# Kernel tuning notes

Measured on AMD Instinct MI355X. Metric: run time of the kernel, lower is better.

Reference implementation:

```python
import jax, jax.numpy as jnp
import numpy as np

N, E = 50000, 800000
IN, HID, H, C = 128, 64, 4, 2
NEG_SLOPE = 0.2


def _gat_layer(h, src, dst, W, al, ar, b, out_dim, residual, resW=None, act='elu'):
    # h: [N, in]; W: [H*out, in]; al/ar: [H, out]; b: [H*out]
    n = h.shape[0]
    feat = (h @ W.T).reshape(n, H, out_dim)            # [N, H, out]
    el = jnp.einsum('nho,ho->nh', feat, al)            # [N, H]
    er = jnp.einsum('nho,ho->nh', feat, ar)            # [N, H]
    e = jax.nn.leaky_relu(el[src] + er[dst], NEG_SLOPE)  # [E, H]
    # segment softmax over incoming edges of each dst node
    emax = jax.ops.segment_max(e, dst, num_segments=n)
    ee = jnp.exp(e - emax[dst])
    denom = jax.ops.segment_sum(ee, dst, num_segments=n)
    alpha = ee / denom[dst]                             # [E, H]
    msg = feat[src] * alpha[:, :, None]                 # [E, H, out]
    rst = jax.ops.segment_sum(msg, dst, num_segments=n)  # [N, H, out]
    if residual == 'id':
        rst = rst + h.reshape(n, H, out_dim)
    elif residual == 'fc':
        rst = rst + (h @ resW.T).reshape(n, H, out_dim)
    rst = rst + b.reshape(1, H, out_dim)
    if act == 'elu':
        rst = jax.nn.elu(rst)
    else:  # softmax over last dim (F.softmax)
        rst = jax.nn.softmax(rst, axis=-1)
    return rst


def setup_inputs() -> dict:
    key = jax.random.key(0)
    ks = jax.random.split(key, 24)
    x = jax.random.normal(ks[0], (N, IN), dtype=jnp.float32)
    src = jax.random.randint(ks[1], (E,), 0, N)
    dst = jax.random.randint(ks[2], (E,), 0, N)
    s = 0.1
    d = {'x': x, 'src': src, 'dst': dst}
    # layer 1: IN -> (H, HID), no residual
    d['W1'] = jax.random.normal(ks[3], (H * HID, IN), dtype=jnp.float32) * s
    d['al1'] = jax.random.normal(ks[4], (H, HID), dtype=jnp.float32) * s
    d['ar1'] = jax.random.normal(ks[5], (H, HID), dtype=jnp.float32) * s
    d['b1'] = jnp.zeros((H * HID,), dtype=jnp.float32)
    # layers 2,3: H*HID -> (H, HID), identity residual
    d['W2'] = jax.random.normal(ks[6], (H * HID, H * HID), dtype=jnp.float32) * s
    d['al2'] = jax.random.normal(ks[7], (H, HID), dtype=jnp.float32) * s
    d['ar2'] = jax.random.normal(ks[8], (H, HID), dtype=jnp.float32) * s
    d['b2'] = jnp.zeros((H * HID,), dtype=jnp.float32)
    d['W3'] = jax.random.normal(ks[9], (H * HID, H * HID), dtype=jnp.float32) * s
    d['al3'] = jax.random.normal(ks[10], (H, HID), dtype=jnp.float32) * s
    d['ar3'] = jax.random.normal(ks[11], (H, HID), dtype=jnp.float32) * s
    d['b3'] = jnp.zeros((H * HID,), dtype=jnp.float32)
    # layer 4: H*HID -> (H, C), linear residual, softmax activation, mean over heads
    d['W4'] = jax.random.normal(ks[12], (H * C, H * HID), dtype=jnp.float32) * s
    d['al4'] = jax.random.normal(ks[13], (H, C), dtype=jnp.float32) * s
    d['ar4'] = jax.random.normal(ks[14], (H, C), dtype=jnp.float32) * s
    d['b4'] = jnp.zeros((H * C,), dtype=jnp.float32)
    d['resW4'] = jax.random.normal(ks[15], (H * C, H * HID), dtype=jnp.float32) * s
    return d


def reference(x, src, dst, W1, al1, ar1, b1, W2, al2, ar2, b2, W3, al3, ar3, b3, W4, al4, ar4, b4, resW4):
    h = _gat_layer(x, src, dst, W1, al1, ar1, b1, HID, 'none', act='elu').reshape(N, H * HID)
    h = _gat_layer(h, src, dst, W2, al2, ar2, b2, HID, 'id', act='elu').reshape(N, H * HID)
    h = _gat_layer(h, src, dst, W3, al3, ar3, b3, HID, 'id', act='elu').reshape(N, H * HID)
    h = _gat_layer(h, src, dst, W4, al4, ar4, b4, C, 'fc', resW=resW4, act='softmax')
    return h.mean(axis=1)  # [N, C]
```

## Files before the change

kernel.cpp:

```cpp
#include <hip/hip_runtime.h>
#include <hip/hip_bf16.h>
#include <math.h>


#define LEAKY_SLOPE 0.2f

typedef __bf16 bf16x8_t __attribute__((ext_vector_type(8)));
typedef float f32x4_t __attribute__((ext_vector_type(4)));
typedef float f32x2_t __attribute__((ext_vector_type(2)));

__device__ __forceinline__ float leaky(float x) { return x > 0.f ? x : LEAKY_SLOPE * x; }
__device__ __forceinline__ float eluf(float x)  { return x > 0.f ? x : expm1f(x); }
__device__ __forceinline__ float bflo(unsigned u) { return __uint_as_float(u << 16); }
__device__ __forceinline__ float bfhi(unsigned u) { return __uint_as_float(u & 0xffff0000u); }

__device__ __forceinline__ int rli(int v, int l) { return __builtin_amdgcn_readlane(v, l); }
__device__ __forceinline__ float rlf(float v, int l) {
  return __uint_as_float((unsigned)__builtin_amdgcn_readlane((int)__float_as_uint(v), l));
}
template <int CTRL>
__device__ __forceinline__ float dpp_add(float x) {
  int t = __builtin_amdgcn_update_dpp(0, (int)__float_as_uint(x), CTRL, 0xf, 0xf, false);
  return x + __uint_as_float((unsigned)t);
}
__device__ __forceinline__ float wsum_dpp(float x) {
  x = dpp_add<0x111>(x);
  x = dpp_add<0x112>(x);
  x = dpp_add<0x114>(x);
  x = dpp_add<0x118>(x);
  x = dpp_add<0x142>(x);
  x = dpp_add<0x143>(x);
  return rlf(x, 63);
}
__device__ __forceinline__ float rowsum_dpp(float x) {
  x = dpp_add<0x111>(x);
  x = dpp_add<0x112>(x);
  x = dpp_add<0x114>(x);
  x = dpp_add<0x118>(x);
  return x;
}
__device__ __forceinline__ float wmax(float v) {
#pragma unroll
  for (int o = 32; o; o >>= 1) v = fmaxf(v, __shfl_xor(v, o));
  return v;
}
__device__ __forceinline__ float wsum_sh(float v) {
#pragma unroll
  for (int o = 32; o; o >>= 1) v += __shfl_xor(v, o);
  return v;
}

__device__ __forceinline__ void edge_fma(f32x2_t& a01, f32x2_t& a23, uint2 u, float4 w) {
  f32x2_t f01 = {bflo(u.x), bfhi(u.x)};
  f32x2_t f23 = {bflo(u.y), bfhi(u.y)};
  f32x2_t w01 = {w.x, w.y};
  f32x2_t w23 = {w.z, w.w};
  a01 = __builtin_elementwise_fma(w01, f01, a01);
  a23 = __builtin_elementwise_fma(w23, f23, a23);
}

__device__ __forceinline__ void gl_lds16(const __hip_bfloat16* g, __bf16* l) {
  __builtin_amdgcn_global_load_lds((const __attribute__((address_space(1))) void*)g,
                                   (__attribute__((address_space(3))) void*)l, 16, 0, 0);
}

__global__ __launch_bounds__(1024) void scan1_k(const int* __restrict__ deg,
                                                int* __restrict__ rowp,
                                                int* __restrict__ bsum, int n) {
  __shared__ int sd[1024];
  int tid = threadIdx.x;
  int i = blockIdx.x * 1024 + tid;
  int v = (i < n) ? deg[i] : 0;
  int x = v;
  sd[tid] = x;
  __syncthreads();
  for (int off = 1; off < 1024; off <<= 1) {
    int t = (tid >= off) ? sd[tid - off] : 0;
    __syncthreads();
    x += t;
    sd[tid] = x;
    __syncthreads();
  }
  if (i < n) rowp[i] = x - v;
  if (tid == 1023) bsum[blockIdx.x] = x;
}

__global__ void scan23_k(const int* __restrict__ bsum, int* __restrict__ rowp, int n, int nb) {
  __shared__ int pref[65];
  int tid = threadIdx.x;
  if (tid < 64) {
    int v = (tid < nb) ? bsum[tid] : 0;
    int x = v;
#pragma unroll
    for (int off = 1; off < 64; off <<= 1) {
      int t = __shfl_up(x, off);
      if (tid >= off) x += t;
    }
    pref[tid] = x - v;
    if (tid == 63) pref[64] = x;
  }
  __syncthreads();
  int i = blockIdx.x * 256 + tid;
  if (i < n) rowp[i] += pref[i >> 10];
  if (i == n) rowp[n] = pref[64];
}

__global__ void scatter_k(const int* __restrict__ src, const int* __restrict__ dst,
                          const int* __restrict__ rowp, int* __restrict__ cur,
                          int* __restrict__ csrc, int e) {
  int i = blockIdx.x * 256 + threadIdx.x;
  if (i < e) {
    int d = dst[i];
    int p = atomicAdd(&cur[d], 1);
    csrc[rowp[d] + p] = src[i];
  }
}

__global__ void cvthist_k(const float* __restrict__ x, const float* __restrict__ W1,
                          const float* __restrict__ W2, const float* __restrict__ W3,
                          const float* __restrict__ W4, const float* __restrict__ rW4,
                          __hip_bfloat16* __restrict__ xb, __hip_bfloat16* __restrict__ W1b,
                          __hip_bfloat16* __restrict__ W2b, __hip_bfloat16* __restrict__ W3b,
                          __hip_bfloat16* __restrict__ Wcatb, int nx,
                          const int* __restrict__ dst, int* __restrict__ deg, int e) {
  int i = blockIdx.x * 256 + threadIdx.x;
  if (i < e) atomicAdd(&deg[dst[i]], 1);
  if (i < nx) { xb[i] = __float2bfloat16(x[i]); return; }
  int j = i - nx;
  if (j < 32768) W1b[j] = __float2bfloat16(W1[j]);
  else if (j < 98304)  { int k = j - 32768;  W2b[k] = __float2bfloat16(W2[k]); }
  else if (j < 163840) { int k = j - 98304;  W3b[k] = __float2bfloat16(W3[k]); }
  else if (j < 165888) { int k = j - 163840; Wcatb[k] = __float2bfloat16(W4[k]); }
  else if (j < 167936) { int k = j - 165888; Wcatb[2048 + k] = __float2bfloat16(rW4[k]); }
}

template <int K>
__global__ __launch_bounds__(256) void gemm_mfma(const __hip_bfloat16* __restrict__ A,
                                                 const __hip_bfloat16* __restrict__ B,
                                                 __hip_bfloat16* __restrict__ featb,
                                                 const float* __restrict__ al,
                                                 const float* __restrict__ ar,
                                                 float* __restrict__ el,
                                                 float* __restrict__ er, int n) {
  __shared__ __bf16 As[128 * 32];
  __shared__ __bf16 Bs[128 * 32];
  const int tid = threadIdx.x;
  const int lane = tid & 63, w = tid >> 6;
  const int tm = lane & 15, tq = lane >> 4;
  const int wm = (w & 1) * 64, wn = (w >> 1) * 64;
  const int r0 = blockIdx.x * 128, c0 = blockIdx.y * 128;

  f32x4_t acc[4][4];
#pragma unroll
  for (int i = 0; i < 4; ++i)
#pragma unroll
    for (int j = 0; j < 4; ++j) acc[i][j] = 0.f;

  const bool interior = (r0 + 128 <= n);
  if (interior) {
    const int srow = w * 32 + (lane >> 2);
    const int scol = (lane & 3) * 8;
    for (int kk = 0; kk < K; kk += 32) {
      __syncthreads();
      const __hip_bfloat16* ga = A + (size_t)(r0 + srow) * K + kk + scol;
      const __hip_bfloat16* gb = B + (size_t)(c0 + srow) * K + kk + scol;
      gl_lds16(ga, As + w * 1024);
      gl_lds16(ga + (size_t)16 * K, As + w * 1024 + 512);
      gl_lds16(gb, Bs + w * 1024);
      gl_lds16(gb + (size_t)16 * K, Bs + w * 1024 + 512);
      __syncthreads();
      bf16x8_t af[4], bfr[4];
#pragma unroll
      for (int i = 0; i < 4; ++i) af[i] = *(const bf16x8_t*)&As[(wm + i * 16 + tm) * 32 + tq * 8];
#pragma unroll
      for (int j = 0; j < 4; ++j) bfr[j] = *(const bf16x8_t*)&Bs[(wn + j * 16 + tm) * 32 + tq * 8];
#pragma unroll
      for (int i = 0; i < 4; ++i)
#pragma unroll
        for (int j = 0; j < 4; ++j)
          acc[i][j] = __builtin_amdgcn_mfma_f32_16x16x32_bf16(af[i], bfr[j], acc[i][j], 0, 0, 0);
    }
  } else {
    const int srow = tid >> 1, sko = (tid & 1) * 16;
    for (int kk = 0; kk < K; kk += 32) {
      uint4 av0 = {0, 0, 0, 0}, av1 = {0, 0, 0, 0};
      int arw = r0 + srow;
      if (arw < n) {
        const uint4* p = (const uint4*)(A + (size_t)arw * K + kk + sko);
        av0 = p[0];
        av1 = p[1];
      }
      const uint4* q = (const uint4*)(B + (size_t)(c0 + srow) * K + kk + sko);
      uint4 bv0 = q[0], bv1 = q[1];
      __syncthreads();
      *(uint4*)&As[srow * 32 + sko] = av0;
      *(uint4*)&As[srow * 32 + sko + 8] = av1;
      *(uint4*)&Bs[srow * 32 + sko] = bv0;
      *(uint4*)&Bs[srow * 32 + sko + 8] = bv1;
      __syncthreads();
      bf16x8_t af[4], bfr[4];
#pragma unroll
      for (int i = 0; i < 4; ++i) af[i] = *(const bf16x8_t*)&As[(wm + i * 16 + tm) * 32 + tq * 8];
#pragma unroll
      for (int j = 0; j < 4; ++j) bfr[j] = *(const bf16x8_t*)&Bs[(wn + j * 16 + tm) * 32 + tq * 8];
#pragma unroll
      for (int i = 0; i < 4; ++i)
#pragma unroll
        for (int j = 0; j < 4; ++j)
          acc[i][j] = __builtin_amdgcn_mfma_f32_16x16x32_bf16(af[i], bfr[j], acc[i][j], 0, 0, 0);
    }
  }

#pragma unroll
  for (int i = 0; i < 4; ++i) {
#pragma unroll
    for (int j = 0; j < 4; ++j) {
      int col = c0 + wn + j * 16 + tm;
      int hh = col >> 6, oo = col & 63;
#pragma unroll
      for (int rr = 0; rr < 4; ++rr) {
        int row = r0 + wm + i * 16 + tq * 4 + rr;
        if (row < n) featb[(size_t)row * 256 + oo * 4 + hh] = __float2bfloat16(acc[i][j][rr]);
      }
    }
  }

  {
    const int hd = (c0 + wn) >> 6;
    float alv[4], arv[4];
#pragma unroll
    for (int j = 0; j < 4; ++j) {
      alv[j] = al[hd * 64 + j * 16 + tm];
      arv[j] = ar[hd * 64 + j * 16 + tm];
    }
#pragma unroll
    for (int i = 0; i < 4; ++i) {
#pragma unroll
      for (int rr = 0; rr < 4; ++rr) {
        float se = acc[i][0][rr] * alv[0] + acc[i][1][rr] * alv[1] +
                   acc[i][2][rr] * alv[2] + acc[i][3][rr] * alv[3];
        float sr2 = acc[i][0][rr] * arv[0] + acc[i][1][rr] * arv[1] +
                    acc[i][2][rr] * arv[2] + acc[i][3][rr] * arv[3];
        se = rowsum_dpp(se);
        sr2 = rowsum_dpp(sr2);
        if (tm == 15) {
          int row = r0 + wm + i * 16 + tq * 4 + rr;
          if (row < n) {
            el[(size_t)row * 4 + hd] = se;
            er[(size_t)row * 4 + hd] = sr2;
          }
        }
      }
    }
  }
}

template <int RES>
__global__ __launch_bounds__(256) void agg64_k(const __hip_bfloat16* __restrict__ featb,
                                               const float* __restrict__ el,
                                               const float* __restrict__ er,
                                               const int* __restrict__ rowp,
                                               const int* __restrict__ csrc,
                                               const __hip_bfloat16* __restrict__ hinb,
                                               const float* __restrict__ bias,
                                               __hip_bfloat16* __restrict__ houtb, int n) {
  __shared__ float wsh[4][256];
  int wv = threadIdx.x >> 6;
  int node = blockIdx.x * 4 + wv;
  int lane = threadIdx.x & 63;
  if (node >= n) return;
  int s0 = rowp[node], s1 = rowp[node + 1];
  int deg = s1 - s0;
  float4 erv = *(const float4*)(er + (size_t)node * 4);
  f32x2_t a01 = {0.f, 0.f}, a23 = {0.f, 0.f};

  if (deg <= 64) {
    int sown = 0;
    float x0 = 0.f, x1 = 0.f, x2 = 0.f, x3 = 0.f;
    if (lane < deg) {
      sown = csrc[s0 + lane];
      float4 e = *(const float4*)(el + (size_t)sown * 4);
      x0 = __expf(leaky(e.x + erv.x));
      x1 = __expf(leaky(e.y + erv.y));
      x2 = __expf(leaky(e.z + erv.z));
      x3 = __expf(leaky(e.w + erv.w));
    }
    float d0 = wsum_dpp(x0), d1 = wsum_dpp(x1), d2 = wsum_dpp(x2), d3 = wsum_dpp(x3);
    float i0 = d0 > 0.f ? 1.f / d0 : 0.f;
    float i1 = d1 > 0.f ? 1.f / d1 : 0.f;
    float i2 = d2 > 0.f ? 1.f / d2 : 0.f;
    float i3 = d3 > 0.f ? 1.f / d3 : 0.f;
    float4 wq = {x0 * i0, x1 * i1, x2 * i2, x3 * i3};
    *(float4*)&wsh[wv][lane * 4] = wq;

    int k = 0;
    for (; k + 8 <= deg; k += 8) {
      int sk0 = rli(sown, k + 0), sk1 = rli(sown, k + 1);
      int sk2 = rli(sown, k + 2), sk3 = rli(sown, k + 3);
      int sk4 = rli(sown, k + 4), sk5 = rli(sown, k + 5);
      int sk6 = rli(sown, k + 6), sk7 = rli(sown, k + 7);
      uint2 u0 = ((const uint2*)(featb + ((size_t)sk0 << 8)))[lane];
      uint2 u1 = ((const uint2*)(featb + ((size_t)sk1 << 8)))[lane];
      uint2 u2 = ((const uint2*)(featb + ((size_t)sk2 << 8)))[lane];
      uint2 u3 = ((const uint2*)(featb + ((size_t)sk3 << 8)))[lane];
      uint2 u4 = ((const uint2*)(featb + ((size_t)sk4 << 8)))[lane];
      uint2 u5 = ((const uint2*)(featb + ((size_t)sk5 << 8)))[lane];
      uint2 u6 = ((const uint2*)(featb + ((size_t)sk6 << 8)))[lane];
      uint2 u7 = ((const uint2*)(featb + ((size_t)sk7 << 8)))[lane];
      edge_fma(a01, a23, u0, *(const float4*)&wsh[wv][(k + 0) * 4]);
      edge_fma(a01, a23, u1, *(const float4*)&wsh[wv][(k + 1) * 4]);
      edge_fma(a01, a23, u2, *(const float4*)&wsh[wv][(k + 2) * 4]);
      edge_fma(a01, a23, u3, *(const float4*)&wsh[wv][(k + 3) * 4]);
      edge_fma(a01, a23, u4, *(const float4*)&wsh[wv][(k + 4) * 4]);
      edge_fma(a01, a23, u5, *(const float4*)&wsh[wv][(k + 5) * 4]);
      edge_fma(a01, a23, u6, *(const float4*)&wsh[wv][(k + 6) * 4]);
      edge_fma(a01, a23, u7, *(const float4*)&wsh[wv][(k + 7) * 4]);
    }
    for (; k + 4 <= deg; k += 4) {
      int sk0 = rli(sown, k + 0), sk1 = rli(sown, k + 1);
      int sk2 = rli(sown, k + 2), sk3 = rli(sown, k + 3);
      uint2 u0 = ((const uint2*)(featb + ((size_t)sk0 << 8)))[lane];
      uint2 u1 = ((const uint2*)(featb + ((size_t)sk1 << 8)))[lane];
      uint2 u2 = ((const uint2*)(featb + ((size_t)sk2 << 8)))[lane];
      uint2 u3 = ((const uint2*)(featb + ((size_t)sk3 << 8)))[lane];
      edge_fma(a01, a23, u0, *(const float4*)&wsh[wv][(k + 0) * 4]);
      edge_fma(a01, a23, u1, *(const float4*)&wsh[wv][(k + 1) * 4]);
      edge_fma(a01, a23, u2, *(const float4*)&wsh[wv][(k + 2) * 4]);
      edge_fma(a01, a23, u3, *(const float4*)&wsh[wv][(k + 3) * 4]);
    }
    for (; k < deg; ++k) {
      int sk = rli(sown, k);
      uint2 u = ((const uint2*)(featb + ((size_t)sk << 8)))[lane];
      edge_fma(a01, a23, u, *(const float4*)&wsh[wv][k * 4]);
    }
  } else {
    float m0 = -INFINITY, m1 = -INFINITY, m2 = -INFINITY, m3 = -INFINITY;
    for (int k = s0 + lane; k < s1; k += 64) {
      int s = csrc[k];
      float4 e = *(const float4*)(el + (size_t)s * 4);
      m0 = fmaxf(m0, leaky(e.x + erv.x));
      m1 = fmaxf(m1, leaky(e.y + erv.y));
      m2 = fmaxf(m2, leaky(e.z + erv.z));
      m3 = fmaxf(m3, leaky(e.w + erv.w));
    }
    m0 = wmax(m0); m1 = wmax(m1); m2 = wmax(m2); m3 = wmax(m3);
    float d0 = 0, d1 = 0, d2 = 0, d3 = 0;
    for (int k = s0 + lane; k < s1; k += 64) {
      int s = csrc[k];
      float4 e = *(const float4*)(el + (size_t)s * 4);
      d0 += __expf(leaky(e.x + erv.x) - m0);
      d1 += __expf(leaky(e.y + erv.y) - m1);
      d2 += __expf(leaky(e.z + erv.z) - m2);
      d3 += __expf(leaky(e.w + erv.w) - m3);
    }
    d0 = wsum_sh(d0); d1 = wsum_sh(d1); d2 = wsum_sh(d2); d3 = wsum_sh(d3);
    float j0 = d0 > 0.f ? 1.f / d0 : 0.f;
    float j1 = d1 > 0.f ? 1.f / d1 : 0.f;
    float j2 = d2 > 0.f ? 1.f / d2 : 0.f;
    float j3 = d3 > 0.f ? 1.f / d3 : 0.f;
    for (int k = s0; k < s1; ++k) {
      int s = csrc[k];
      float4 e = *(const float4*)(el + (size_t)s * 4);
      float4 wk;
      wk.x = __expf(leaky(e.x + erv.x) - m0) * j0;
      wk.y = __expf(leaky(e.y + erv.y) - m1) * j1;
      wk.z = __expf(leaky(e.z + erv.z) - m2) * j2;
      wk.w = __expf(leaky(e.w + erv.w) - m3) * j3;
      uint2 u = ((const uint2*)(featb + ((size_t)s << 8)))[lane];
      edge_fma(a01, a23, u, wk);
    }
  }

  size_t base = (size_t)node * 256;
  float v0 = a01[0] + bias[lane];
  float v1 = a01[1] + bias[64 + lane];
  float v2 = a23[0] + bias[128 + lane];
  float v3 = a23[1] + bias[192 + lane];
  if (RES) {
    v0 += __bfloat162float(hinb[base + lane]);
    v1 += __bfloat162float(hinb[base + 64 + lane]);
    v2 += __bfloat162float(hinb[base + 128 + lane]);
    v3 += __bfloat162float(hinb[base + 192 + lane]);
  }
  houtb[base + lane]       = __float2bfloat16(eluf(v0));
  houtb[base + 64 + lane]  = __float2bfloat16(eluf(v1));
  houtb[base + 128 + lane] = __float2bfloat16(eluf(v2));
  houtb[base + 192 + lane] = __float2bfloat16(eluf(v3));
}

__global__ __launch_bounds__(256) void l4mfma_k(const __hip_bfloat16* __restrict__ hb,
                                                const __hip_bfloat16* __restrict__ Wcat,
                                                const float* __restrict__ al4,
                                                const float* __restrict__ ar4,
                                                float* __restrict__ feat4,
                                                float* __restrict__ res4,
                                                float* __restrict__ el4,
                                                float* __restrict__ er4, int n) {
  int wid = blockIdx.x * 4 + (threadIdx.x >> 6);
  int n16 = (n + 15) >> 4;
  if (wid >= n16) return;
  int lane = threadIdx.x & 63;
  int tm = lane & 15, tq = lane >> 4;
  int row = wid * 16 + tm;
  int rowc = row < n ? row : n - 1;
  const __hip_bfloat16* ap = hb + (size_t)rowc * 256 + tq * 8;
  const __hip_bfloat16* bp = Wcat + (size_t)tm * 256 + tq * 8;
  f32x4_t acc = {0.f, 0.f, 0.f, 0.f};
#pragma unroll
  for (int k = 0; k < 8; ++k) {
    bf16x8_t af = *(const bf16x8_t*)(ap + k * 32);
    bf16x8_t bf = *(const bf16x8_t*)(bp + k * 32);
    acc = __builtin_amdgcn_mfma_f32_16x16x32_bf16(af, bf, acc, 0, 0, 0);
  }
  float* dstp = (tm < 8) ? feat4 : res4;
  int cc = tm & 7;
  float a4 = (tm < 8) ? al4[tm] : 0.f;
  float r4 = (tm < 8) ? ar4[tm] : 0.f;
#pragma unroll
  for (int r = 0; r < 4; ++r) {
    int node = wid * 16 + tq * 4 + r;
    float te = acc[r] * a4;
    float tr = acc[r] * r4;
    te += __shfl_xor(te, 1);
    tr += __shfl_xor(tr, 1);
    if (node < n) {
      dstp[(size_t)node * 8 + cc] = acc[r];
      if (tm < 8 && (tm & 1) == 0) {
        el4[(size_t)node * 4 + (tm >> 1)] = te;
        er4[(size_t)node * 4 + (tm >> 1)] = tr;
      }
    }
  }
}

__global__ __launch_bounds__(256) void agg4_k(const float* __restrict__ feat4,
                                              const float* __restrict__ el4,
                                              const float* __restrict__ er4,
                                              const int* __restrict__ rowp,
                                              const int* __restrict__ csrc,
                                              const float* __restrict__ res4,
                                              const float* __restrict__ b4,
                                              float* __restrict__ out, int n) {
  __shared__ int ssh[4][64];
  __shared__ float wsh[4][256];
  int wv = threadIdx.x >> 6;
  int node = blockIdx.x * 4 + wv;
  int lane = threadIdx.x & 63;
  if (node >= n) return;
  int s0 = rowp[node], s1 = rowp[node + 1];
  int deg = s1 - s0;
  float4 erv = *(const float4*)(er4 + (size_t)node * 4);
  float acc = 0.f;
  float scale = 1.f;
  int p = lane & 7, hh = p >> 1;

  if (deg <= 64) {
    int sown = 0;
    float x0 = 0.f, x1 = 0.f, x2 = 0.f, x3 = 0.f;
    if (lane < deg) {
      sown = csrc[s0 + lane];
      float4 e = *(const float4*)(el4 + (size_t)sown * 4);
      x0 = __expf(leaky(e.x + erv.x));
      x1 = __expf(leaky(e.y + erv.y));
      x2 = __expf(leaky(e.z + erv.z));
      x3 = __expf(leaky(e.w + erv.w));
    }
    float d0 = wsum_dpp(x0), d1 = wsum_dpp(x1), d2 = wsum_dpp(x2), d3 = wsum_dpp(x3);
    float i0 = d0 > 0.f ? 1.f / d0 : 0.f;
    float i1 = d1 > 0.f ? 1.f / d1 : 0.f;
    float i2 = d2 > 0.f ? 1.f / d2 : 0.f;
    float i3 = d3 > 0.f ? 1.f / d3 : 0.f;
    scale = (hh == 0) ? i0 : (hh == 1) ? i1 : (hh == 2) ? i2 : i3;
    ssh[wv][lane] = sown;
    float4 wq = {x0, x1, x2, x3};
    *(float4*)&wsh[wv][lane * 4] = wq;
    int g = lane >> 3;
    int nt = (deg + 7) >> 3;
    for (int t = 0; t < nt; ++t) {
      int k = g + t * 8;
      bool ok = k < deg;
      int kk = k & 63;
      int sk = ssh[wv][kk];
      float wk = wsh[wv][kk * 4 + hh];
      if (ok) acc = fmaf(wk, feat4[(size_t)sk * 8 + p], acc);
    }
    acc += __shfl_xor(acc, 8);
    acc += __shfl_xor(acc, 16);
    acc += __shfl_xor(acc, 32);
  } else {
    float m0 = -INFINITY, m1 = -INFINITY, m2 = -INFINITY, m3 = -INFINITY;
    for (int k = s0 + lane; k < s1; k += 64) {
      int s = csrc[k];
      float4 e = *(const float4*)(el4 + (size_t)s * 4);
      m0 = fmaxf(m0, leaky(e.x + erv.x));
      m1 = fmaxf(m1, leaky(e.y + erv.y));
      m2 = fmaxf(m2, leaky(e.z + erv.z));
      m3 = fmaxf(m3, leaky(e.w + erv.w));
    }
    m0 = wmax(m0); m1 = wmax(m1); m2 = wmax(m2); m3 = wmax(m3);
    float d0 = 0, d1 = 0, d2 = 0, d3 = 0;
    for (int k = s0 + lane; k < s1; k += 64) {
      int s = csrc[k];
      float4 e = *(const float4*)(el4 + (size_t)s * 4);
      d0 += __expf(leaky(e.x + erv.x) - m0);
      d1 += __expf(leaky(e.y + erv.y) - m1);
      d2 += __expf(leaky(e.z + erv.z) - m2);
      d3 += __expf(leaky(e.w + erv.w) - m3);
    }
    d0 = wsum_sh(d0); d1 = wsum_sh(d1); d2 = wsum_sh(d2); d3 = wsum_sh(d3);
    float i0 = d0 > 0.f ? 1.f / d0 : 0.f;
    float i1 = d1 > 0.f ? 1.f / d1 : 0.f;
    float i2 = d2 > 0.f ? 1.f / d2 : 0.f;
    float i3 = d3 > 0.f ? 1.f / d3 : 0.f;
    for (int k = s0; k < s1; ++k) {
      int s = csrc[k];
      float4 e = *(const float4*)(el4 + (size_t)s * 4);
      float w0 = __expf(leaky(e.x + erv.x) - m0) * i0;
      float w1 = __expf(leaky(e.y + erv.y) - m1) * i1;
      float w2 = __expf(leaky(e.z + erv.z) - m2) * i2;
      float w3 = __expf(leaky(e.w + erv.w) - m3) * i3;
      float wk = (hh == 0) ? w0 : (hh == 1) ? w1 : (hh == 2) ? w2 : w3;
      if (lane < 8) acc = fmaf(wk, feat4[(size_t)s * 8 + p], acc);
    }
  }

  float v = 0.f;
  if (lane < 8) v = acc * scale + res4[(size_t)node * 8 + lane] + b4[lane];
  float pv = __shfl_xor(v, 1);
  float mx = fmaxf(v, pv);
  float ex = __expf(v - mx);
  float sm = ex + __shfl_xor(ex, 1);
  float pr = ex / sm;
  float t = pr + __shfl_xor(pr, 2);
  t += __shfl_xor(t, 4);
  if (lane < 2) out[(size_t)node * 2 + lane] = t * 0.25f;
}

extern "C" void kernel_launch(void* const* d_in, const int* in_sizes, int n_in,
                              void* d_out, int out_size, void* d_ws, size_t ws_size,
                              hipStream_t stream) {
  const float* x   = (const float*)d_in[0];
  const int* src   = (const int*)d_in[1];
  const int* dst   = (const int*)d_in[2];
  const float* W1  = (const float*)d_in[3];
  const float* al1 = (const float*)d_in[4];
  const float* ar1 = (const float*)d_in[5];
  const float* b1  = (const float*)d_in[6];
  const float* W2  = (const float*)d_in[7];
  const float* al2 = (const float*)d_in[8];
  const float* ar2 = (const float*)d_in[9];
  const float* b2  = (const float*)d_in[10];
  const float* W3  = (const float*)d_in[11];
  const float* al3 = (const float*)d_in[12];
  const float* ar3 = (const float*)d_in[13];
  const float* b3  = (const float*)d_in[14];
  const float* W4  = (const float*)d_in[15];
  const float* al4 = (const float*)d_in[16];
  const float* ar4 = (const float*)d_in[17];
  const float* b4  = (const float*)d_in[18];
  const float* rW4 = (const float*)d_in[19];
  float* out = (float*)d_out;

  const int n = in_sizes[0] / 128;
  const int e = in_sizes[1];

  char* ws = (char*)d_ws;
  auto alloc = [&](size_t bytes) -> char* {
    char* p = ws;
    ws += (bytes + 255) & ~(size_t)255;
    return p;
  };
  __hip_bfloat16* featb = (__hip_bfloat16*)alloc((size_t)n * 256 * 2);
  __hip_bfloat16* h1b   = (__hip_bfloat16*)alloc((size_t)n * 256 * 2);
  __hip_bfloat16* h2b   = (__hip_bfloat16*)alloc((size_t)n * 256 * 2);
  __hip_bfloat16* h3b   = (__hip_bfloat16*)alloc((size_t)n * 256 * 2);
  __hip_bfloat16* xb    = (__hip_bfloat16*)alloc((size_t)n * 128 * 2);
  __hip_bfloat16* W1b   = (__hip_bfloat16*)alloc((size_t)256 * 128 * 2);
  __hip_bfloat16* W2b   = (__hip_bfloat16*)alloc((size_t)256 * 256 * 2);
  __hip_bfloat16* W3b   = (__hip_bfloat16*)alloc((size_t)256 * 256 * 2);
  __hip_bfloat16* Wcatb = (__hip_bfloat16*)alloc((size_t)16 * 256 * 2);
  float* el    = (float*)alloc((size_t)n * 4 * 4);
  float* er    = (float*)alloc((size_t)n * 4 * 4);
  float* feat4 = (float*)alloc((size_t)n * 8 * 4);
  float* res4  = (float*)alloc((size_t)n * 8 * 4);
  float* el4   = (float*)alloc((size_t)n * 4 * 4);
  float* er4   = (float*)alloc((size_t)n * 4 * 4);
  int* deg     = (int*)alloc((size_t)2 * n * 4);
  int* cur     = deg + n;
  int* rowp    = (int*)alloc((size_t)(n + 1) * 4);
  int* csrc    = (int*)alloc((size_t)e * 4);
  int nb_scan  = (n + 1023) / 1024;
  int* bsum    = (int*)alloc((size_t)(nb_scan + 1) * 4);

  (void)hipMemsetAsync(deg, 0, (size_t)2 * n * 4, stream);

  int nx = n * 128;
  cvthist_k<<<(nx + 167936 + 255) / 256, 256, 0, stream>>>(x, W1, W2, W3, W4, rW4, xb, W1b,
                                                           W2b, W3b, Wcatb, nx, dst, deg, e);
  scan1_k<<<nb_scan, 1024, 0, stream>>>(deg, rowp, bsum, n);
  scan23_k<<<(n + 256) / 256, 256, 0, stream>>>(bsum, rowp, n, nb_scan);
  scatter_k<<<(e + 255) / 256, 256, 0, stream>>>(src, dst, rowp, cur, csrc, e);

  dim3 ggrid((n + 127) / 128, 2);
  int nb4 = (n + 3) / 4;

  gemm_mfma<128><<<ggrid, 256, 0, stream>>>(xb, W1b, featb, al1, ar1, el, er, n);
  agg64_k<0><<<nb4, 256, 0, stream>>>(featb, el, er, rowp, csrc, nullptr, b1, h1b, n);
  gemm_mfma<256><<<ggrid, 256, 0, stream>>>(h1b, W2b, featb, al2, ar2, el, er, n);
  agg64_k<1><<<nb4, 256, 0, stream>>>(featb, el, er, rowp, csrc, h1b, b2, h2b, n);
  gemm_mfma<256><<<ggrid, 256, 0, stream>>>(h2b, W3b, featb, al3, ar3, el, er, n);
  agg64_k<1><<<nb4, 256, 0, stream>>>(featb, el, er, rowp, csrc, h2b, b3, h3b, n);
  int n16 = (n + 15) / 16;
  l4mfma_k<<<(n16 + 3) / 4, 256, 0, stream>>>(h3b, Wcatb, al4, ar4, feat4, res4, el4, er4, n);
  agg4_k<<<nb4, 256, 0, stream>>>(feat4, el4, er4, rowp, csrc, res4, b4, out, n);
}
```

Before: 498.8 us.

## Split wave into two half-waves gathering 16-byte rows in aggregation; reduce layer-4 via DPP

```diff
diff --git a/kernel.cpp b/kernel.cpp
--- a/kernel.cpp
+++ b/kernel.cpp
@@ -14,7 +14,6 @@
 __device__ __forceinline__ float bflo(unsigned u) { return __uint_as_float(u << 16); }
 __device__ __forceinline__ float bfhi(unsigned u) { return __uint_as_float(u & 0xffff0000u); }
 
-__device__ __forceinline__ int rli(int v, int l) { return __builtin_amdgcn_readlane(v, l); }
 __device__ __forceinline__ float rlf(float v, int l) {
   return __uint_as_float((unsigned)__builtin_amdgcn_readlane((int)__float_as_uint(v), l));
 }
@@ -50,11 +49,20 @@
   return v;
 }
 
+__device__ __forceinline__ void pair_fma(f32x2_t& c001, f32x2_t& c023, f32x2_t& c101,
+                                         f32x2_t& c123, uint4 u, float4 w) {
+  f32x2_t w01 = {w.x, w.y}, w23 = {w.z, w.w};
+  f32x2_t f;
+  f[0] = bflo(u.x); f[1] = bfhi(u.x); c001 = __builtin_elementwise_fma(w01, f, c001);
+  f[0] = bflo(u.y); f[1] = bfhi(u.y); c023 = __builtin_elementwise_fma(w23, f, c023);
+  f[0] = bflo(u.z); f[1] = bfhi(u.z); c101 = __builtin_elementwise_fma(w01, f, c101);
+  f[0] = bflo(u.w); f[1] = bfhi(u.w); c123 = __builtin_elementwise_fma(w23, f, c123);
+}
+
 __device__ __forceinline__ void edge_fma(f32x2_t& a01, f32x2_t& a23, uint2 u, float4 w) {
-  f32x2_t f01 = {bflo(u.x), bfhi(u.x)};
-  f32x2_t f23 = {bflo(u.y), bfhi(u.y)};
-  f32x2_t w01 = {w.x, w.y};
-  f32x2_t w23 = {w.z, w.w};
+  f32x2_t f01, f23, w01 = {w.x, w.y}, w23 = {w.z, w.w};
+  f01[0] = bflo(u.x); f01[1] = bfhi(u.x);
+  f23[0] = bflo(u.y); f23[1] = bfhi(u.y);
   a01 = __builtin_elementwise_fma(w01, f01, a01);
   a23 = __builtin_elementwise_fma(w23, f23, a23);
 }
@@ -265,6 +273,7 @@
                                                const float* __restrict__ bias,
                                                __hip_bfloat16* __restrict__ houtb, int n) {
   __shared__ float wsh[4][256];
+  __shared__ int ssh[4][64];
   int wv = threadIdx.x >> 6;
   int node = blockIdx.x * 4 + wv;
   int lane = threadIdx.x & 63;
@@ -272,7 +281,6 @@
   int s0 = rowp[node], s1 = rowp[node + 1];
   int deg = s1 - s0;
   float4 erv = *(const float4*)(er + (size_t)node * 4);
-  f32x2_t a01 = {0.f, 0.f}, a23 = {0.f, 0.f};
 
   if (deg <= 64) {
     int sown = 0;
@@ -292,48 +300,65 @@
     float i3 = d3 > 0.f ? 1.f / d3 : 0.f;
     float4 wq = {x0 * i0, x1 * i1, x2 * i2, x3 * i3};
     *(float4*)&wsh[wv][lane * 4] = wq;
-
+    ssh[wv][lane] = sown;
+
+    const int half = lane >> 5, sub = lane & 31;
+    f32x2_t c001 = {0.f, 0.f}, c023 = {0.f, 0.f};
+    f32x2_t c101 = {0.f, 0.f}, c123 = {0.f, 0.f};
     int k = 0;
     for (; k + 8 <= deg; k += 8) {
-      int sk0 = rli(sown, k + 0), sk1 = rli(sown, k + 1);
-      int sk2 = rli(sown, k + 2), sk3 = rli(sown, k + 3);
-      int sk4 = rli(sown, k + 4), sk5 = rli(sown, k + 5);
-      int sk6 = rli(sown, k + 6), sk7 = rli(sown, k + 7);
-      uint2 u0 = ((const uint2*)(featb + ((size_t)sk0 << 8)))[lane];
-      uint2 u1 = ((const uint2*)(featb + ((size_t)sk1 << 8)))[lane];
-      uint2 u2 = ((const uint2*)(featb + ((size_t)sk2 << 8)))[lane];
-      uint2 u3 = ((const uint2*)(featb + ((size_t)sk3 << 8)))[lane];
-      uint2 u4 = ((const uint2*)(featb + ((size_t)sk4 << 8)))[lane];
-      uint2 u5 = ((const uint2*)(featb + ((size_t)sk5 << 8)))[lane];
-      uint2 u6 = ((const uint2*)(featb + ((size_t)sk6 << 8)))[lane];
-      uint2 u7 = ((const uint2*)(featb + ((size_t)sk7 << 8)))[lane];
-      edge_fma(a01, a23, u0, *(const float4*)&wsh[wv][(k + 0) * 4]);
-      edge_fma(a01, a23, u1, *(const float4*)&wsh[wv][(k + 1) * 4]);
-      edge_fma(a01, a23, u2, *(const float4*)&wsh[wv][(k + 2) * 4]);
-      edge_fma(a01, a23, u3, *(const float4*)&wsh[wv][(k + 3) * 4]);
-      edge_fma(a01, a23, u4, *(const float4*)&wsh[wv][(k + 4) * 4]);
-      edge_fma(a01, a23, u5, *(const float4*)&wsh[wv][(k + 5) * 4]);
-      edge_fma(a01, a23, u6, *(const float4*)&wsh[wv][(k + 6) * 4]);
-      edge_fma(a01, a23, u7, *(const float4*)&wsh[wv][(k + 7) * 4]);
-    }
-    for (; k + 4 <= deg; k += 4) {
-      int sk0 = rli(sown, k + 0), sk1 = rli(sown, k + 1);
-      int sk2 = rli(sown, k + 2), sk3 = rli(sown, k + 3);
-      uint2 u0 = ((const uint2*)(featb + ((size_t)sk0 << 8)))[lane];
-      uint2 u1 = ((const uint2*)(featb + ((size_t)sk1 << 8)))[lane];
-      uint2 u2 = ((const uint2*)(featb + ((size_t)sk2 << 8)))[lane];
-      uint2 u3 = ((const uint2*)(featb + ((size_t)sk3 << 8)))[lane];
-      edge_fma(a01, a23, u0, *(const float4*)&wsh[wv][(k + 0) * 4]);
-      edge_fma(a01, a23, u1, *(const float4*)&wsh[wv][(k + 1) * 4]);
-      edge_fma(a01, a23, u2, *(const float4*)&wsh[wv][(k + 2) * 4]);
-      edge_fma(a01, a23, u3, *(const float4*)&wsh[wv][(k + 3) * 4]);
-    }
-    for (; k < deg; ++k) {
-      int sk = rli(sown, k);
-      uint2 u = ((const uint2*)(featb + ((size_t)sk << 8)))[lane];
-      edge_fma(a01, a23, u, *(const float4*)&wsh[wv][k * 4]);
-    }
+      int ke = k + half;
+      int sk0 = ssh[wv][ke], sk1 = ssh[wv][ke + 2];
+      int sk2 = ssh[wv][ke + 4], sk3 = ssh[wv][ke + 6];
+      uint4 u0 = ((const uint4*)(featb + ((size_t)sk0 << 8)))[sub];
+      uint4 u1 = ((const uint4*)(featb + ((size_t)sk1 << 8)))[sub];
+      uint4 u2 = ((const uint4*)(featb + ((size_t)sk2 << 8)))[sub];
+      uint4 u3 = ((const uint4*)(featb + ((size_t)sk3 << 8)))[sub];
+      float4 w0 = *(const float4*)&wsh[wv][(ke)*4];
+      float4 w1 = *(const float4*)&wsh[wv][(ke + 2) * 4];
+      float4 w2 = *(const float4*)&wsh[wv][(ke + 4) * 4];
+      float4 w3 = *(const float4*)&wsh[wv][(ke + 6) * 4];
+      pair_fma(c001, c023, c101, c123, u0, w0);
+      pair_fma(c001, c023, c101, c123, u1, w1);
+      pair_fma(c001, c023, c101, c123, u2, w2);
+      pair_fma(c001, c023, c101, c123, u3, w3);
+    }
+    for (; k < deg; k += 2) {
+      int ke = k + half;
+      int sk = ssh[wv][ke];
+      uint4 u = ((const uint4*)(featb + ((size_t)sk << 8)))[sub];
+      float4 w = *(const float4*)&wsh[wv][ke * 4];
+      pair_fma(c001, c023, c101, c123, u, w);
+    }
+    c001[0] += __shfl_xor(c001[0], 32); c001[1] += __shfl_xor(c001[1], 32);
+    c023[0] += __shfl_xor(c023[0], 32); c023[1] += __shfl_xor(c023[1], 32);
+    c101[0] += __shfl_xor(c101[0], 32); c101[1] += __shfl_xor(c101[1], 32);
+    c123[0] += __shfl_xor(c123[0], 32); c123[1] += __shfl_xor(c123[1], 32);
+
+    size_t base = (size_t)node * 256;
+    int hA = half * 2, hB = hA + 1;
+    int colo = sub * 2;
+    float pa0 = half ? c023[0] : c001[0];
+    float pa1 = half ? c123[0] : c101[0];
+    float pb0 = half ? c023[1] : c001[1];
+    float pb1 = half ? c123[1] : c101[1];
+    float vA0 = pa0 + bias[hA * 64 + colo];
+    float vA1 = pa1 + bias[hA * 64 + colo + 1];
+    float vB0 = pb0 + bias[hB * 64 + colo];
+    float vB1 = pb1 + bias[hB * 64 + colo + 1];
+    if (RES) {
+      unsigned rA = *(const unsigned*)(hinb + base + hA * 64 + colo);
+      unsigned rB = *(const unsigned*)(hinb + base + hB * 64 + colo);
+      vA0 += bflo(rA); vA1 += bfhi(rA);
+      vB0 += bflo(rB); vB1 += bfhi(rB);
+    }
+    __hip_bfloat162 oA, oB;
+    oA.x = __float2bfloat16(eluf(vA0)); oA.y = __float2bfloat16(eluf(vA1));
+    oB.x = __float2bfloat16(eluf(vB0)); oB.y = __float2bfloat16(eluf(vB1));
+    *(__hip_bfloat162*)(houtb + base + hA * 64 + colo) = oA;
+    *(__hip_bfloat162*)(houtb + base + hB * 64 + colo) = oB;
   } else {
+    f32x2_t a01 = {0.f, 0.f}, a23 = {0.f, 0.f};
     float m0 = -INFINITY, m1 = -INFINITY, m2 = -INFINITY, m3 = -INFINITY;
     for (int k = s0 + lane; k < s1; k += 64) {
       int s = csrc[k];
@@ -369,23 +394,22 @@
       uint2 u = ((const uint2*)(featb + ((size_t)s << 8)))[lane];
       edge_fma(a01, a23, u, wk);
     }
-  }
-
-  size_t base = (size_t)node * 256;
-  float v0 = a01[0] + bias[lane];
-  float v1 = a01[1] + bias[64 + lane];
-  float v2 = a23[0] + bias[128 + lane];
-  float v3 = a23[1] + bias[192 + lane];
-  if (RES) {
-    v0 += __bfloat162float(hinb[base + lane]);
-    v1 += __bfloat162float(hinb[base + 64 + lane]);
-    v2 += __bfloat162float(hinb[base + 128 + lane]);
-    v3 += __bfloat162float(hinb[base + 192 + lane]);
-  }
-  houtb[base + lane]       = __float2bfloat16(eluf(v0));
-  houtb[base + 64 + lane]  = __float2bfloat16(eluf(v1));
-  houtb[base + 128 + lane] = __float2bfloat16(eluf(v2));
-  houtb[base + 192 + lane] = __float2bfloat16(eluf(v3));
+    size_t base = (size_t)node * 256;
+    float v0 = a01[0] + bias[lane];
+    float v1 = a01[1] + bias[64 + lane];
+    float v2 = a23[0] + bias[128 + lane];
+    float v3 = a23[1] + bias[192 + lane];
+    if (RES) {
+      v0 += __bfloat162float(hinb[base + lane]);
+      v1 += __bfloat162float(hinb[base + 64 + lane]);
+      v2 += __bfloat162float(hinb[base + 128 + lane]);
+      v3 += __bfloat162float(hinb[base + 192 + lane]);
+    }
+    houtb[base + lane]       = __float2bfloat16(eluf(v0));
+    houtb[base + 64 + lane]  = __float2bfloat16(eluf(v1));
+    houtb[base + 128 + lane] = __float2bfloat16(eluf(v2));
+    houtb[base + 192 + lane] = __float2bfloat16(eluf(v3));
+  }
 }
 
 __global__ __launch_bounds__(256) void l4mfma_k(const __hip_bfloat16* __restrict__ hb,
@@ -441,8 +465,6 @@
                                               const float* __restrict__ res4,
                                               const float* __restrict__ b4,
                                               float* __restrict__ out, int n) {
-  __shared__ int ssh[4][64];
-  __shared__ float wsh[4][256];
   int wv = threadIdx.x >> 6;
   int node = blockIdx.x * 4 + wv;
   int lane = threadIdx.x & 63;
@@ -450,9 +472,7 @@
   int s0 = rowp[node], s1 = rowp[node + 1];
   int deg = s1 - s0;
   float4 erv = *(const float4*)(er4 + (size_t)node * 4);
-  float acc = 0.f;
-  float scale = 1.f;
-  int p = lane & 7, hh = p >> 1;
+  float v = 0.f;
 
   if (deg <= 64) {
     int sown = 0;
@@ -466,28 +486,31 @@
       x3 = __expf(leaky(e.w + erv.w));
     }
     float d0 = wsum_dpp(x0), d1 = wsum_dpp(x1), d2 = wsum_dpp(x2), d3 = wsum_dpp(x3);
-    float i0 = d0 > 0.f ? 1.f / d0 : 0.f;
-    float i1 = d1 > 0.f ? 1.f / d1 : 0.f;
-    float i2 = d2 > 0.f ? 1.f / d2 : 0.f;
-    float i3 = d3 > 0.f ? 1.f / d3 : 0.f;
-    scale = (hh == 0) ? i0 : (hh == 1) ? i1 : (hh == 2) ? i2 : i3;
-    ssh[wv][lane] = sown;
-    float4 wq = {x0, x1, x2, x3};
-    *(float4*)&wsh[wv][lane * 4] = wq;
-    int g = lane >> 3;
-    int nt = (deg + 7) >> 3;
-    for (int t = 0; t < nt; ++t) {
-      int k = g + t * 8;
-      bool ok = k < deg;
-      int kk = k & 63;
-      int sk = ssh[wv][kk];
-      float wk = wsh[wv][kk * 4 + hh];
-      if (ok) acc = fmaf(wk, feat4[(size_t)sk * 8 + p], acc);
-    }
-    acc += __shfl_xor(acc, 8);
-    acc += __shfl_xor(acc, 16);
-    acc += __shfl_xor(acc, 32);
+    float w0 = x0 * (d0 > 0.f ? 1.f / d0 : 0.f);
+    float w1 = x1 * (d1 > 0.f ? 1.f / d1 : 0.f);
+    float w2 = x2 * (d2 > 0.f ? 1.f / d2 : 0.f);
+    float w3 = x3 * (d3 > 0.f ? 1.f / d3 : 0.f);
+    float4 f0 = {0, 0, 0, 0}, f1 = {0, 0, 0, 0};
+    if (lane < deg) {
+      const float4* fp = (const float4*)(feat4 + (size_t)sown * 8);
+      f0 = fp[0];
+      f1 = fp[1];
+    }
+    float t0 = w0 * f0.x, t1 = w0 * f0.y;
+    float t2 = w1 * f0.z, t3 = w1 * f0.w;
+    float t4 = w2 * f1.x, t5 = w2 * f1.y;
+    float t6 = w3 * f1.z, t7 = w3 * f1.w;
+    t0 = wsum_dpp(t0); t1 = wsum_dpp(t1); t2 = wsum_dpp(t2); t3 = wsum_dpp(t3);
+    t4 = wsum_dpp(t4); t5 = wsum_dpp(t5); t6 = wsum_dpp(t6); t7 = wsum_dpp(t7);
+    int p = lane & 7;
+    float s = t0;
+    s = (p == 1) ? t1 : s; s = (p == 2) ? t2 : s; s = (p == 3) ? t3 : s;
+    s = (p == 4) ? t4 : s; s = (p == 5) ? t5 : s; s = (p == 6) ? t6 : s;
+    s = (p == 7) ? t7 : s;
+    if (lane < 8) v = s + res4[(size_t)node * 8 + lane] + b4[lane];
   } else {
+    int p = lane & 7, hh = p >> 1;
+    float acc = 0.f;
     float m0 = -INFINITY, m1 = -INFINITY, m2 = -INFINITY, m3 = -INFINITY;
     for (int k = s0 + lane; k < s1; k += 64) {
       int s = csrc[k];
@@ -522,10 +545,9 @@
       float wk = (hh == 0) ? w0 : (hh == 1) ? w1 : (hh == 2) ? w2 : w3;
       if (lane < 8) acc = fmaf(wk, feat4[(size_t)s * 8 + p], acc);
     }
-  }
-
-  float v = 0.f;
-  if (lane < 8) v = acc * scale + res4[(size_t)node * 8 + lane] + b4[lane];
+    if (lane < 8) v = acc + res4[(size_t)node * 8 + lane] + b4[lane];
+  }
+
   float pv = __shfl_xor(v, 1);
   float mx = fmaxf(v, pv);
   float ex = __expf(v - mx);
```

Result: no change. 496.9 us (-0.4%).
